# Kernel tuning notes

Measured on AMD Instinct MI355X. Metric: run time of the kernel, lower is better.

## Reference

```python
import jax, jax.numpy as jnp
import numpy as np

N, B, S = 2048, 8, 256          # nodes, graphs, nodes-per-graph (sorted equal segments)
D_IN, HID, HEADS, HC = 4096, 512, 8, 64
E, K, L, A = 32768, 8, 2, 5      # edges, rwse steps, gps layers, actions
EPS = 1e-5


def layernorm(x, g, b):
    mu = x.mean(-1, keepdims=True)
    var = ((x - mu) ** 2).mean(-1, keepdims=True)
    return (x - mu) * jax.lax.rsqrt(var + EPS) * g + b


def gelu(x):
    return jax.nn.gelu(x, approximate=False)  # torch nn.GELU default (erf)


def segment_softmax(logits, seg, num_segments):
    mx = jax.ops.segment_max(logits, seg, num_segments=num_segments)
    ex = jnp.exp(logits - mx[seg])
    den = jax.ops.segment_sum(ex, seg, num_segments=num_segments)
    return ex / (den[seg] + 1e-16)


def gatv2(h, src, dst, ea, Wl, bl, Wr, br, We, att, bias):
    # PyG GATv2Conv: x_j from lin_l(src), x_i from lin_r(dst), + lin_edge(edge_attr)
    xl = (h @ Wl + bl).reshape(N, HEADS, HC)
    xr = (h @ Wr + br).reshape(N, HEADS, HC)
    em = (ea @ We).reshape(-1, HEADS, HC)
    m = xl[src] + xr[dst] + em                     # [E+N, HEADS, HC]
    m = jnp.where(m > 0, m, 0.2 * m)               # leaky_relu(0.2)
    logit = (m * att).sum(-1)                      # [E+N, HEADS]
    alpha = segment_softmax(logit, dst, N)
    out = jax.ops.segment_sum(alpha[:, :, None] * xl[src], dst, num_segments=N)
    return out.reshape(N, HEADS * HC) + bias


def mha(xg, inW, inb, outW, outb):
    # xg: [B, S, HID]; block-diagonal per-graph attention (torch loop over batch ids)
    qkv = xg @ inW + inb
    q, k, v = jnp.split(qkv, 3, axis=-1)
    hsplit = lambda t: t.reshape(B, S, HEADS, HC).transpose(0, 2, 1, 3)
    q, k, v = hsplit(q), hsplit(k), hsplit(v)
    att = jax.nn.softmax(jnp.einsum('bhqd,bhkd->bhqk', q, k) / np.sqrt(HC), axis=-1)
    o = jnp.einsum('bhqk,bhkd->bhqd', att, v).transpose(0, 2, 1, 3).reshape(B, S, HID)
    return o @ outW + outb


def forward(x, edge_attr, rwse_W, rwse_b, rwse_g, rwse_bt, np_W, np_b, np_g, np_bt,
            gat_Wl, gat_bl, gat_Wr, gat_br, gat_We, gat_att, gat_bias,
            n1_g, n1_b, mha_inW, mha_inb, mha_outW, mha_outb, alpha_p,
            n2_g, n2_b, ffn_W1, ffn_b1, ffn_W2, ffn_b2, n3_g, n3_b,
            ah_W1, ah_b1, ah_g, ah_bt, ah_W2, ah_b2,
            edge_index, current_node_idx):
    src0, dst0 = edge_index[0], edge_index[1]
    # --- RWSE: diag of k-step random-walk transition powers ---
    adj = jnp.zeros((N, N), x.dtype).at[src0, dst0].set(1.0)
    deg = adj.sum(1, keepdims=True)
    T = adj / jnp.where(deg > 0, deg, 1.0)
    def step(cur, _):
        cur = cur @ T
        return cur, jnp.diagonal(cur)
    _, diags = jax.lax.scan(step, jnp.eye(N, dtype=x.dtype), None, length=K)
    rwse = diags.T                                  # [N, K]
    r = gelu(layernorm(rwse @ rwse_W + rwse_b, rwse_g, rwse_bt))
    h = gelu(layernorm(jnp.concatenate([x, r], -1) @ np_W + np_b, np_g, np_bt))
    # --- self loops for GATv2 (add_self_loops=True, edge_attr fill='mean') ---
    ar = jnp.arange(N)
    src = jnp.concatenate([src0, ar])
    dst = jnp.concatenate([dst0, ar])
    ea = jnp.concatenate([edge_attr, jnp.broadcast_to(edge_attr.mean(0), (N, 2))], 0)
    for i in range(L):
        local = gatv2(h, src, dst, ea, gat_Wl[i], gat_bl[i], gat_Wr[i], gat_br[i],
                      gat_We[i], gat_att[i], gat_bias[i])
        local = layernorm(local, n1_g[i], n1_b[i])
        g = mha(h.reshape(B, S, HID), mha_inW[i], mha_inb[i],
                mha_outW[i], mha_outb[i]).reshape(N, HID)
        g = layernorm(g, n2_g[i], n2_b[i])
        a = jax.nn.sigmoid(alpha_p[i])
        comb = a * local + (1.0 - a) * g
        ff = gelu(comb @ ffn_W1[i] + ffn_b1[i]) @ ffn_W2[i] + ffn_b2[i]
        h = layernorm(comb + ff, n3_g[i], n3_b[i])
    emb = h[current_node_idx]
    z = gelu(layernorm(emb @ ah_W1 + ah_b1, ah_g, ah_bt))
    logits = z @ ah_W2 + ah_b2
    return logits, jax.nn.softmax(logits, axis=-1)


def setup_inputs() -> dict:
    key = jax.random.key(0)
    ks = iter(jax.random.split(key, 64))
    def w(shape, fan_in):
        return jax.random.normal(next(ks), shape, jnp.float32) / np.sqrt(fan_in)
    H4 = HID // 4
    inp = {
        'x': jax.random.normal(next(ks), (N, D_IN), jnp.float32),
        'edge_attr': jax.random.normal(next(ks), (E, 2), jnp.float32),
        'rwse_W': w((K, H4), K), 'rwse_b': jnp.zeros(H4),
        'rwse_g': jnp.ones(H4), 'rwse_bt': jnp.zeros(H4),
        'np_W': w((D_IN + H4, HID), D_IN + H4), 'np_b': jnp.zeros(HID),
        'np_g': jnp.ones(HID), 'np_bt': jnp.zeros(HID),
        'gat_Wl': w((L, HID, HID), HID), 'gat_bl': jnp.zeros((L, HID)),
        'gat_Wr': w((L, HID, HID), HID), 'gat_br': jnp.zeros((L, HID)),
        'gat_We': w((L, 2, HID), 2), 'gat_att': w((L, HEADS, HC), HC),
        'gat_bias': jnp.zeros((L, HID)),
        'n1_g': jnp.ones((L, HID)), 'n1_b': jnp.zeros((L, HID)),
        'mha_inW': w((L, HID, 3 * HID), HID), 'mha_inb': jnp.zeros((L, 3 * HID)),
        'mha_outW': w((L, HID, HID), HID), 'mha_outb': jnp.zeros((L, HID)),
        'alpha_p': jnp.full((L,), 0.5, jnp.float32),
        'n2_g': jnp.ones((L, HID)), 'n2_b': jnp.zeros((L, HID)),
        'ffn_W1': w((L, HID, 4 * HID), HID), 'ffn_b1': jnp.zeros((L, 4 * HID)),
        'ffn_W2': w((L, 4 * HID, HID), 4 * HID), 'ffn_b2': jnp.zeros((L, HID)),
        'n3_g': jnp.ones((L, HID)), 'n3_b': jnp.zeros((L, HID)),
        'ah_W1': w((HID, HID), HID), 'ah_b1': jnp.zeros(HID),
        'ah_g': jnp.ones(HID), 'ah_bt': jnp.zeros(HID),
        'ah_W2': w((HID, A), HID), 'ah_b2': jnp.zeros(A),
        'edge_index': jax.random.randint(next(ks), (2, E), 0, N),
        'current_node_idx': 100,
    }
    return inp


def reference(x, edge_attr, rwse_W, rwse_b, rwse_g, rwse_bt, np_W, np_b, np_g, np_bt,
              gat_Wl, gat_bl, gat_Wr, gat_br, gat_We, gat_att, gat_bias,
              n1_g, n1_b, mha_inW, mha_inb, mha_outW, mha_outb, alpha_p,
              n2_g, n2_b, ffn_W1, ffn_b1, ffn_W2, ffn_b2, n3_g, n3_b,
              ah_W1, ah_b1, ah_g, ah_bt, ah_W2, ah_b2,
              edge_index, current_node_idx):
    return forward(x, edge_attr, rwse_W, rwse_b, rwse_g, rwse_bt, np_W, np_b, np_g, np_bt,
                   gat_Wl, gat_bl, gat_Wr, gat_br, gat_We, gat_att, gat_bias,
                   n1_g, n1_b, mha_inW, mha_inb, mha_outW, mha_outb, alpha_p,
                   n2_g, n2_b, ffn_W1, ffn_b1, ffn_W2, ffn_b2, n3_g, n3_b,
                   ah_W1, ah_b1, ah_g, ah_bt, ah_W2, ah_b2,
                   edge_index, current_node_idx)
```

## Files before the change

kernel.cpp:

```cpp
#include <hip/hip_runtime.h>
#include <math.h>

constexpr int NODES = 2048;
constexpr int BG = 8;
constexpr int SG = 256;
constexpr int DIN = 4096;
constexpr int NHEAD = 8;
constexpr int EDGES = 32768;
constexpr int ACT_N = 5;
constexpr int H4C = 128;
constexpr int ECAP = 192;
constexpr int SCAP = 96;
constexpr int QS = 2560;
constexpr int NC = 512;

typedef unsigned short u16;
typedef unsigned int u32;
typedef unsigned long long u64;
typedef short short8 __attribute__((ext_vector_type(8)));
typedef float f32x4 __attribute__((ext_vector_type(4)));

__device__ __forceinline__ float wave_sum(float v) {
#pragma unroll
  for (int o = 32; o; o >>= 1) v += __shfl_xor(v, o);
  return v;
}
__device__ __forceinline__ float wave_max(float v) {
#pragma unroll
  for (int o = 32; o; o >>= 1) v = fmaxf(v, __shfl_xor(v, o));
  return v;
}
__device__ __forceinline__ float blk_sum(float v, float* sh) {
  v = wave_sum(v);
  int nw = blockDim.x >> 6;
  __syncthreads();
  if ((threadIdx.x & 63) == 0) sh[threadIdx.x >> 6] = v;
  __syncthreads();
// ... 5 lines not shown
  v = wave_max(v);
  int nw = blockDim.x >> 6;
  __syncthreads();
  if ((threadIdx.x & 63) == 0) sh[threadIdx.x >> 6] = v;
  __syncthreads();
  float m = sh[0];
  for (int k = 1; k < nw; k++) m = fmaxf(m, sh[k]);
  return m;
}
__device__ __forceinline__ float gelu_f(float x) {
  return 0.5f * x * (1.f + erff(x * 0.70710678118654752f));
}
__device__ __forceinline__ u16 f2bf(float x) {
  u32 u = __float_as_uint(x);
  return (u16)((u + 0x7FFFu + ((u >> 16) & 1u)) >> 16);
}
__device__ __forceinline__ float bf2f(u16 h) { return __uint_as_float(((u32)h) << 16); }
__device__ __forceinline__ void split2(float v, u16* ph, u16* pl) {
  u16 h = f2bf(v);
  *ph = h;
  *pl = f2bf(v - bf2f(h));
}

__global__ void build_graph(const int* __restrict__ ei, u32* __restrict__ bits,
                            int* __restrict__ scnt, int* __restrict__ slist,
                            int* __restrict__ cnt, int* __restrict__ elist) {
  int e = blockIdx.x * 256 + threadIdx.x;
  if (e < EDGES) {
    int s = ei[e], d = ei[EDGES + e];
    u32 m = 1u << (d & 31);
    u32 old = atomicOr(&bits[s * 64 + (d >> 5)], m);
    if (!(old & m)) {
      int p = atomicAdd(&scnt[s], 1);
      if (p < SCAP) slist[s * SCAP + p] = d;
    }
    int p2 = atomicAdd(&cnt[d], 1);
    if (p2 < ECAP) elist[(size_t)d * ECAP + p2] = e;
  } else if (e < EDGES + NODES) {
    int d = e - EDGES;
    int p = atomicAdd(&cnt[d], 1);
    if (p < ECAP) elist[(size_t)d * ECAP + p] = e;
  }
}

__global__ __launch_bounds__(256) void spmm_sq(const int* __restrict__ scnt,
                                               const int* __restrict__ slist,
                                               float* __restrict__ P2,
                                               float* __restrict__ rwse) {
  int i = blockIdx.x, t = threadIdx.x;
  __shared__ float row[NODES];
  for (int c = t; c < NODES; c += 256) row[c] = 0.f;
  __syncthreads();
  int di = min(scnt[i], SCAP);
  float wi = di > 0 ? 1.f / (float)di : 0.f;
  for (int jj = 0; jj < di; jj++) {
    int j = slist[i * SCAP + jj];
    int dj = min(scnt[j], SCAP);
    if (dj == 0) continue;
    float w = wi / (float)dj;
    for (int kk = t; kk < dj; kk += 256) atomicAdd(&row[slist[j * SCAP + kk]], w);
  }
  __syncthreads();
  for (int c = t; c < NODES; c += 256) {
    float v = row[c];
// ... 78 lines not shown
  int self = (bits[i * 64 + (i >> 5)] >> (i & 31)) & 1;
  rwse[(size_t)i * 8 + 0] = (self && deg > 0) ? 1.f / (float)deg : 0.f;
#pragma unroll
  for (int v = 0; v < 4; v++) {
    float s = 0.f;
    for (int js = 0; js < 8; js++) s += pbuf[((size_t)js * NODES + i) * 4 + v];
    rwse[(size_t)i * 8 + 4 + v] = s;
  }
}

__device__ __forceinline__ void splitA8(const float* __restrict__ p, short8& h8,
                                        short8& l8) {
  float4 v0 = *(const float4*)p;
  float4 v1 = *(const float4*)(p + 4);
  float v[8] = {v0.x, v0.y, v0.z, v0.w, v1.x, v1.y, v1.z, v1.w};
#pragma unroll
  for (int i = 0; i < 8; i++) {
    u16 h = f2bf(v[i]);
    h8[i] = (short)h;
    l8[i] = (short)f2bf(v[i] - bf2f(h));
  }
}

__global__ void conv_split(const float* __restrict__ src, u16* __restrict__ Ah,
                           u16* __restrict__ Al, int total8, int Ksrc,
                           int dstStride, int colOff) {
  int u = blockIdx.x * 256 + threadIdx.x;
  if (u >= total8) return;
  int idx = u * 8;
  int m = idx / Ksrc, k = idx - m * Ksrc;
  short8 h8, l8;
  splitA8(src + idx, h8, l8);
  size_t o = (size_t)m * dstStride + colOff + k;
  *(short8*)(Ah + o) = h8;
  *(short8*)(Al + o) = l8;
}

struct PackArgs {
  const float* src[13];
  u64 offU[13];
  u64 cumU[14];
  int N[13];
  int srcStride[13];
  int gnTot[13];
  int ntOff[13];
};

__global__ __launch_bounds__(256) void pack_all(PackArgs pa, u16* __restrict__ Bh,
                                                u16* __restrict__ Bl) {
  u64 total = pa.cumU[13];
  for (u64 u = (u64)blockIdx.x * 256 + threadIdx.x; u < total;
       u += (u64)gridDim.x * 256) {
    int s = 0;
    while (u >= pa.cumU[s + 1]) s++;
    u64 ur = u - pa.cumU[s];
    int lr = (int)(ur & 15);
    int g = (int)((ur >> 4) & 3);
    int ks = (int)((ur >> 6) & 1);
    int j = (int)((ur >> 7) & 3);
    u64 rest = ur >> 9;
    int Nseg = pa.N[s] >> 6;
    int nt = (int)(rest % (u32)Nseg);
    int ktile = (int)(rest / (u32)Nseg);
    int k0 = (ktile << 6) | (ks << 5) | (g << 3);
    int n = (nt << 6) | (j << 4) | lr;
    const float* src = pa.src[s];
    int stride = pa.srcStride[s];
    u64 fiU = pa.offU[s] +
              ((((u64)ktile * pa.gnTot[s] + pa.ntOff[s] + nt) * 8 + j * 2 + ks) * 64 +
               g * 16 + lr);
    short8 h8, l8;
#pragma unroll
    for (int e = 0; e < 8; e++) {
      float v = src[(size_t)(k0 + e) * stride + n];
      u16 h = f2bf(v);
      h8[e] = (short)h;
      l8[e] = (short)f2bf(v - bf2f(h));
    }
// ... 177 lines not shown
    v1 += x[(size_t)s * MN + base + 256 + t];
  }
  if (gbias) { v0 += gbias[t]; v1 += gbias[t + 256]; }
  if (res) { v0 += res[base + t]; v1 += res[base + 256 + t]; }
  __shared__ float sh[8];
  float s = blk_sum(v0 + v1, sh);
  float mu = s * (1.f / 512.f);
  float d0 = v0 - mu, d1 = v1 - mu;
  float var = blk_sum(d0 * d0 + d1 * d1, sh) * (1.f / 512.f);
  float rstd = rsqrtf(var + 1e-5f);
  float o0 = d0 * rstd * g[t] + b[t];
  float o1 = d1 * rstd * g[t + 256] + b[t + 256];
  if (do_gelu) { o0 = gelu_f(o0); o1 = gelu_f(o1); }
  if (mix) {
    float a = 1.f / (1.f + expf(-ap[l]));
    o0 = a * mix[base + t] + (1.f - a) * o0;
    o1 = a * mix[base + 256 + t] + (1.f - a) * o1;
  }
  if (y) { y[base + t] = o0; y[base + 256 + t] = o1; }
  if (yh) {
    split2(o0, yh + base + t, yl + base + t);
    split2(o1, yh + base + 256 + t, yl + base + 256 + t);
  }
}

__global__ void build_cbias(const float* __restrict__ bl, const float* __restrict__ br,
                            const float* __restrict__ inb, float* __restrict__ cb) {
  int i = blockIdx.x * 256 + threadIdx.x;
  if (i >= QS) return;
  cb[i] = i < 512 ? bl[i] : (i < 1024 ? br[i - 512] : inb[i - 1024]);
}

__global__ void build_rowmap(const int* __restrict__ cni, const int* __restrict__ cnt,
                             const int* __restrict__ elist, const int* __restrict__ ei,
                             int* __restrict__ rowmap) {
  int t = blockIdx.x * 256 + threadIdx.x;
  if (t >= NC) return;
  int i = cni[0];
  if (t < 256) {
    rowmap[t] = ((i >> 8) << 8) + t;
  } else {
    int p = t - 256;
    int m = min(cnt[i], ECAP);
    int v = 0;
    if (p < m) {
      int eid = elist[(size_t)i * ECAP + p];
      v = eid < EDGES ? ei[eid] : i;
    }
    rowmap[t] = v;
  }
}

__global__ void ea_reduce(const float* __restrict__ ea, float* __restrict__ sums) {
  int tid = blockIdx.x * blockDim.x + threadIdx.x;
  int stride = gridDim.x * blockDim.x;
  float s0 = 0.f, s1 = 0.f;
  for (int e = tid; e < EDGES; e += stride) { s0 += ea[2 * e]; s1 += ea[2 * e + 1]; }
  s0 = wave_sum(s0);
  s1 = wave_sum(s1);
  if ((threadIdx.x & 63) == 0) { atomicAdd(&sums[0], s0); atomicAdd(&sums[1], s1); }
}

__global__ __launch_bounds__(512) void gat_kernel(
    const float* __restrict__ hb, const int* __restrict__ rowmap,
    const float* __restrict__ eattr, const float* __restrict__ easum,
    const float* __restrict__ We, const float* __restrict__ att,
    const float* __restrict__ bias, const int* __restrict__ cnt,
    const int* __restrict__ elist, const int* __restrict__ ei,
    const float* __restrict__ n1g, const float* __restrict__ n1b,
    float* __restrict__ out) {
  int i = rowmap[blockIdx.x];
  int tid = threadIdx.x;
  int h = tid >> 6, c = tid & 63;
  int m_cnt = cnt[i];
  if (m_cnt > ECAP) m_cnt = ECAP;
  const float inv_e = 1.f / (float)EDGES;
  float we0 = We[tid], we1 = We[512 + tid];
  float attv = att[tid];
  float xrv = hb[(size_t)i * QS + 512 + tid];
  float ea_m0 = easum[0] * inv_e, ea_m1 = easum[1] * inv_e;
  __shared__ float logits[NHEAD][ECAP];
  __shared__ float sh[8];
  const int* el = elist + (size_t)i * ECAP;
// ... 174 lines not shown
  int kb = blockIdx.y;
  const float* xr = h1c + (size_t)(cni[0] & 255) * 512 + kb * 64;
  if (t < 64) xv[t] = xr[t];
  __syncthreads();
  int b = blockIdx.x;
  int isq = b < 8;
  int nl = t & 63;
  int n = (b & 7) * 64 + nl;
  int seg = t >> 6;
  const float* W = isq ? inW : Wr;
  int ldW = isq ? 1536 : 512;
  float acc = 0.f;
  const float* Wp = W + (size_t)(kb * 64 + seg * 16) * ldW + n;
#pragma unroll
  for (int k = 0; k < 16; k++) acc += xv[seg * 16 + k] * Wp[(size_t)k * ldW];
  red[seg][nl] = acc;
  __syncthreads();
  if (t < 64) {
    part[(size_t)kb * 1024 + (isq ? 0 : 512) + (b & 7) * 64 + t] =
        red[0][t] + red[1][t] + red[2][t] + red[3][t];
  }
}

__global__ void reduce_qxr(const float* __restrict__ part,
                           const float* __restrict__ inb,
                           const float* __restrict__ br,
                           float* __restrict__ qrow, float* __restrict__ xrrow) {
  int n = blockIdx.x * 256 + threadIdx.x;
  float s = n < 512 ? inb[n] : br[n - 512];
  for (int k = 0; k < 8; k++) s += part[(size_t)k * 1024 + n];
  if (n < 512) qrow[n] = s;
  else xrrow[n - 512] = s;
}

__global__ void row_reduce(const float* __restrict__ part, int KB, int N,
                           const float* __restrict__ bias,
                           float* __restrict__ out, int act) {
  int n = blockIdx.x * 256 + threadIdx.x;
  if (n >= N) return;
  float s = bias[n];
  for (int k = 0; k < KB; k++) s += part[(size_t)k * N + n];
  if (act) s = gelu_f(s);
  out[n] = s;
}

__global__ __launch_bounds__(512) void gat_l2(
    const float* __restrict__ xlc, const float* __restrict__ xrrow,
    const int* __restrict__ cni,
    const float* __restrict__ eattr, const float* __restrict__ easum,
    const float* __restrict__ We, const float* __restrict__ att,
    const float* __restrict__ bias, const int* __restrict__ cnt,
    const int* __restrict__ elist,
    const float* __restrict__ n1g, const float* __restrict__ n1b,
    float* __restrict__ local_row) {
  int i = cni[0];
  int tid = threadIdx.x;
  int h = tid >> 6, c = tid & 63;
  int m_cnt = cnt[i];
  if (m_cnt > ECAP) m_cnt = ECAP;
  const float inv_e = 1.f / (float)EDGES;
  float we0 = We[tid], we1 = We[512 + tid];
  float attv = att[tid];
  float xrv = xrrow[tid];
  float ea_m0 = easum[0] * inv_e, ea_m1 = easum[1] * inv_e;
  __shared__ float logits[NHEAD][ECAP];
  __shared__ float sh[8];
  const int* el = elist + (size_t)i * ECAP;
  for (int e = 0; e < m_cnt; e++) {
    int eid = el[e];
    float a0, a1;
    if (eid < EDGES) { a0 = eattr[2 * eid]; a1 = eattr[2 * eid + 1]; }
    else { a0 = ea_m0; a1 = ea_m1; }
    float mval = xlc[(size_t)(256 + e) * 512 + tid] + xrv + a0 * we0 + a1 * we1;
    mval = mval > 0.f ? mval : 0.2f * mval;
    float lg = wave_sum(mval * attv);
    if (c == 0) logits[h][e] = lg;
  }
  float mx = -1e30f;
  for (int e = c; e < m_cnt; e += 64) mx = fmaxf(mx, logits[h][e]);
  mx = wave_max(mx);
  float den = 0.f;
  for (int e = c; e < m_cnt; e += 64) den += expf(logits[h][e] - mx);
  den = wave_sum(den) + 1e-16f;
  float acc = 0.f;
  for (int e = 0; e < m_cnt; e++) {
    float alpha = expf(logits[h][e] - mx) / den;
    acc += alpha * xlc[(size_t)(256 + e) * 512 + tid];
  }
  float v = acc + bias[tid];
  float mu = blk_sum(v, sh) * (1.f / 512.f);
  float d = v - mu;
  float var = blk_sum(d * d, sh) * (1.f / 512.f);
  local_row[tid] = d * rsqrtf(var + 1e-5f) * n1g[tid] + n1b[tid];
}

__global__ __launch_bounds__(256) void mha_row(const float* __restrict__ qrow,
                                               const float* __restrict__ kv,
                                               float* __restrict__ attO_row) {
  __shared__ float q[64];
  __shared__ float p[SG];
  __shared__ float sh[8];
  __shared__ float red[4][64];
  int h = blockIdx.x, t = threadIdx.x;
  if (t < 64) q[t] = qrow[h * 64 + t];
  __syncthreads();
  const float* kr = kv + (size_t)t * 1024 + h * 64;
  float s = 0.f;
#pragma unroll 8
  for (int c2 = 0; c2 < 64; c2++) s += q[c2] * kr[c2];
  s *= 0.125f;
  float m = blk_max(s, sh);
  float e = __expf(s - m);
  p[t] = e;
  float den = blk_sum(e, sh);
  int c = t & 63, seg = t >> 6;
  float o = 0.f;
  for (int j = seg * 64; j < seg * 64 + 64; j++)
    o += p[j] * kv[(size_t)j * 1024 + 512 + h * 64 + c];
  red[seg][c] = o;
  __syncthreads();
  if (t < 64)
    attO_row[h * 64 + t] = (red[0][t] + red[1][t] + red[2][t] + red[3][t]) / den;
}

__global__ __launch_bounds__(512) void comb_l2(const float* __restrict__ part, int KB,
                                               const float* __restrict__ bias,
                                               const float* __restrict__ local_row,
                                               const float* __restrict__ ap, int l,
                                               const float* __restrict__ g,
                                               const float* __restrict__ b,
                                               float* __restrict__ comb_row) {
  __shared__ float sh[8];
  int t = threadIdx.x;
  float v = bias[t];
  for (int k = 0; k < KB; k++) v += part[(size_t)k * 512 + t];
  float mu = blk_sum(v, sh) * (1.f / 512.f);
  float d = v - mu;
  float var = blk_sum(d * d, sh) * (1.f / 512.f);
  float o = d * rsqrtf(var + 1e-5f) * g[t] + b[t];
  float a = 1.f / (1.f + expf(-ap[l]));
  comb_row[t] = a * local_row[t] + (1.f - a) * o;
}

__global__ __launch_bounds__(512) void final_l2(const float* __restrict__ part, int KB,
                                                const float* __restrict__ bias,
                                                const float* __restrict__ comb_row,
                                                const float* __restrict__ g,
                                                const float* __restrict__ b,
                                                float* __restrict__ hrow) {
  __shared__ float sh[8];
  int t = threadIdx.x;
  float v = bias[t] + comb_row[t];
  for (int k = 0; k < KB; k++) v += part[(size_t)k * 512 + t];
  float mu = blk_sum(v, sh) * (1.f / 512.f);
  float d = v - mu;
  float var = blk_sum(d * d, sh) * (1.f / 512.f);
  hrow[t] = d * rsqrtf(var + 1e-5f) * g[t] + b[t];
}

__global__ __launch_bounds__(512) void head_finish(
    const float* __restrict__ part, int KB,
    const float* __restrict__ b1,
    const float* __restrict__ g, const float* __restrict__ bt,
    const float* __restrict__ W2, const float* __restrict__ b2,
    float* __restrict__ out) {
  __shared__ float sh[8];
  __shared__ float lg[ACT_N];
  int t = threadIdx.x;
  float v = b1[t];
  for (int k = 0; k < KB; k++) v += part[(size_t)k * 512 + t];
  float mu = blk_sum(v, sh) * (1.f / 512.f);
  float d = v - mu;
  float var = blk_sum(d * d, sh) * (1.f / 512.f);
  float z = gelu_f(d * rsqrtf(var + 1e-5f) * g[t] + bt[t]);
  for (int a = 0; a < ACT_N; a++) {
    float s = blk_sum(z * W2[t * ACT_N + a], sh);
    if (t == 0) lg[a] = s + b2[a];
  }
  __syncthreads();
  if (t == 0) {
// ... 53 lines not shown
  const int* edge_index = (const int*)d_in[38];
  const int* cni        = (const int*)d_in[39];
  (void)in_sizes; (void)n_in; (void)out_size; (void)ws_size;

  char* wsp = (char*)d_ws;
  size_t off = 0;
  auto alloc = [&](size_t bytes) -> char* {
    char* p = wsp + off;
    off += (bytes + 255) & ~(size_t)255;
    return p;
  };
  const size_t NNb = (size_t)NODES * NODES * 4;
  char* arena = alloc(3 * NNb);
  float* P2 = (float*)arena;
  float* P3 = (float*)(arena + NNb);
  float* P4 = (float*)(arena + 2 * NNb);
  u16* Axh = (u16*)arena;
  u16* Axl = (u16*)(arena + 17301504);
  float* hbig = (float*)arena;
  float* partC = (float*)(arena + 22020096);
  const u64 SEG_NP = 2162688ull;
  const u64 SEG_L0 = 3670016ull;
  const u64 L1_OFF = SEG_NP + SEG_L0;
  const u64 KV1_OFF = L1_OFF + 262144ull;
  const u64 PTOT = KV1_OFF + 524288ull;
  u16* Bh = (u16*)alloc(PTOT * 2);
  u16* Bl = (u16*)alloc(PTOT * 2);
  float* partNP = (float*)alloc((size_t)6 * NODES * 512 * 4);
  float* rwse = (float*)alloc((size_t)NODES * 8 * 4);
  u16* h1h = (u16*)alloc((size_t)NODES * 512 * 2);
  u16* h1l = (u16*)alloc((size_t)NODES * 512 * 2);
  u16* attOh = (u16*)alloc((size_t)NODES * 512 * 2);
  u16* attOl = (u16*)alloc((size_t)NODES * 512 * 2);
  u16* combh = (u16*)alloc((size_t)NC * 512 * 2);
  u16* combl = (u16*)alloc((size_t)NC * 512 * 2);
  u16* ffmh = (u16*)alloc((size_t)NC * 2048 * 2);
  u16* ffml = (u16*)alloc((size_t)NC * 2048 * 2);
  u16* h1ch = (u16*)alloc((size_t)NC * 512 * 2);
  u16* h1cl = (u16*)alloc((size_t)NC * 512 * 2);
  float* h1c  = (float*)alloc((size_t)NC * 512 * 4);
  float* gout = (float*)alloc((size_t)NC * 512 * 4);
  float* comb = (float*)alloc((size_t)NC * 512 * 4);
  float* kvbuf = (float*)alloc((size_t)256 * 1024 * 4);
  float* cb   = (float*)alloc((size_t)QS * 4);
  float* rows = (float*)alloc(4096 * 4);
  float* pv1 = (float*)alloc((size_t)32 * 2048 * 4);
  char* zbase = alloc((size_t)NODES * 64 * 4 + NODES * 4 + NODES * 4 + 256);
  u32* bits  = (u32*)zbase;
  int* scnt  = (int*)(zbase + (size_t)NODES * 64 * 4);
  int* cnt   = (int*)(zbase + (size_t)NODES * 64 * 4 + NODES * 4);
  float* easum = (float*)(zbase + (size_t)NODES * 64 * 4 + NODES * 8);
  size_t zbytes = (size_t)NODES * 64 * 4 + NODES * 8 + 256;
  int* slist = (int*)alloc((size_t)NODES * SCAP * 4);
  int* elist = (int*)alloc((size_t)NODES * ECAP * 4);
  int* rmap  = (int*)alloc((size_t)NC * 4);
  float* pbuf  = (float*)alloc((size_t)8 * NODES * 4 * 4);
  float* qrow = rows, *xrrow = rows + 512, *local_row = rows + 1024;
  float* attO_row = rows + 1536, *comb_row = rows + 2560;
  float* midrow = rows + 3072 - 1024;
  float* midrow2 = (float*)alloc(2048 * 4);
  float* hrow = rows + 3584;

  hipMemsetAsync(zbase, 0, zbytes, stream);
  build_graph<<<(EDGES + NODES + 255) / 256, 256, 0, stream>>>(edge_index, bits,
                                                               scnt, slist, cnt,
                                                               elist);
  ea_reduce<<<64, 256, 0, stream>>>(eattr, easum);
  build_rowmap<<<2, 256, 0, stream>>>(cni, cnt, elist, edge_index, rmap);

  spmm_sq<<<NODES, 256, 0, stream>>>(scnt, slist, P2, rwse);
  spmm_gather<<<NODES, 256, 0, stream>>>(scnt, slist, P2, P3, rwse, 2);
  spmm_gather<<<NODES, 256, 0, stream>>>(scnt, slist, P3, P4, rwse, 3);
  diag_tiled<<<dim3(NODES / 64, 8), 256, 0, stream>>>(P2, P3, P4, pbuf);
  diag_reduce<<<NODES / 256, 256, 0, stream>>>(pbuf, bits, scnt, rwse);
  conv_split<<<NODES * DIN / 8 / 256, 256, 0, stream>>>(x, Axh, Axl,
                                                        NODES * DIN / 8, DIN, 4224, 0);
  rwse_proj<<<NODES, 128, 0, stream>>>(rwse, rwse_W, rwse_b, rwse_g, rwse_bt,
                                       Axh, Axl);

  PackArgs pa;
  u64 uc = 0;
  int si = 0;
  auto seg = [&](const float* src, int K, int N, int stride, u64 offElems,
                 int gnTot, int ntOff) {
    pa.src[si] = src; pa.offU[si] = offElems / 8; pa.cumU[si] = uc;
    pa.N[si] = N; pa.srcStride[si] = stride; pa.gnTot[si] = gnTot;
    pa.ntOff[si] = ntOff;
    uc += (u64)K * N / 8; si++;
  };
  seg(np_W, 4224, 512, 512, 0, 8, 0);
  seg(gat_Wl, 512, 512, 512, SEG_NP, 40, 0);
  seg(gat_Wr, 512, 512, 512, SEG_NP, 40, 8);
  seg(mha_inW, 512, 1536, 1536, SEG_NP, 40, 16);
  seg(mha_outW, 512, 512, 512, SEG_NP + 1310720, 8, 0);
  seg(ffn_W1, 512, 2048, 2048, SEG_NP + 1572864, 32, 0);
  seg(ffn_W2, 2048, 512, 512, SEG_NP + 2621440, 8, 0);
  seg(gat_Wl + 512 * 512, 512, 512, 512, L1_OFF, 8, 0);
  seg(mha_inW + 512 * 1536 + 512, 512, 1024, 1536, KV1_OFF, 16, 0);
  for (int s2 = si; s2 <= 13; s2++) pa.cumU[s2] = uc;
  pack_all<<<2048, 256, 0, stream>>>(pa, Bh, Bl);
  build_cbias<<<(QS + 255) / 256, 256, 0, stream>>>(gat_bl, gat_br, mha_inb, cb);

  gemm_s<<<dim3(256, 6), 256, 0, stream>>>(Axh, Axl, 4224, Bh, Bl,
                                           nullptr, nullptr, nullptr, nullptr,
                                           NODES, 4224, 512, 0, 704, partNP,
                                           nullptr);
  ln512<<<NODES, 256, 0, stream>>>(partNP, 6, NODES, np_b, nullptr, nullptr,
                                   nullptr, 0, np_g, np_bt, nullptr, h1h, h1l, 1);

  {
    const u64 lb = SEG_NP;
    gemm_s<<<dim3(1280), 256, 0, stream>>>(h1h, h1l, 512, Bh + lb, Bl + lb,
                                           hbig, nullptr, nullptr, cb,
                                           NODES, 512, QS, 0, 512, nullptr,
                                           nullptr);
    gat_kernel<<<NC, 512, 0, stream>>>(hbig, rmap, eattr, easum, gat_We, gat_att,
                                       gat_bias, cnt, elist, edge_index,
                                       n1_g, n1_b, gout);
    mha_mfma<<<BG * NHEAD * 4, 256, 0, stream>>>(hbig + 1024, attOh, attOl);
    gemm_s<<<dim3(64, 2), 256, 0, stream>>>(attOh, attOl, 512, Bh + lb + 1310720,
                                            Bl + lb + 1310720, nullptr, nullptr,
                                            nullptr, nullptr, NC, 512, 512, 0, 256,
                                            partC, rmap);
    ln512<<<NC, 256, 0, stream>>>(partC, 2, NC, mha_outb, nullptr, gout, alpha_p,
                                  0, n2_g, n2_b, comb, combh, combl, 0);
    gemm_s<<<dim3(256), 256, 0, stream>>>(combh, combl, 512, Bh + lb + 1572864,
                                          Bl + lb + 1572864, nullptr, ffmh, ffml,
                                          ffn_b1, NC, 512, 2048, 1, 512, nullptr,
                                          nullptr);
    gemm_s<<<dim3(64, 4), 256, 0, stream>>>(ffmh, ffml, 2048, Bh + lb + 2621440,
                                            Bl + lb + 2621440, nullptr, nullptr,
                                            nullptr, nullptr, NC, 2048, 512, 0,
                                            512, partC, nullptr);
    ln512<<<NC, 256, 0, stream>>>(partC, 4, NC, ffn_b2, comb, nullptr, nullptr, 0,
                                  n3_g, n3_b, h1c, h1ch, h1cl, 0);
  }

  {
    float* xlc = gout;
    gemm_s<<<dim3(64), 256, 0, stream>>>(h1ch, h1cl, 512, Bh + L1_OFF, Bl + L1_OFF,
                                         xlc, nullptr, nullptr, gat_bl + 512,
                                         NC, 512, 512, 0, 512, nullptr, nullptr);
    gemm_s<<<dim3(64), 256, 0, stream>>>(h1ch, h1cl, 512, Bh + KV1_OFF, Bl + KV1_OFF,
                                         kvbuf, nullptr, nullptr,
                                         mha_inb + 1536 + 512, 256, 512, 1024, 0,
                                         512, nullptr, nullptr);
    gemv_qxr<<<dim3(16, 8), 256, 0, stream>>>(h1c, cni, mha_inW + 512 * 1536,
                                              gat_Wr + 512 * 512, pv1);
    reduce_qxr<<<4, 256, 0, stream>>>(pv1, mha_inb + 1536, gat_br + 512, qrow,
                                      xrrow);
    gat_l2<<<1, 512, 0, stream>>>(xlc, xrrow, cni, eattr, easum, gat_We + 1024,
                                  gat_att + 512, gat_bias + 512, cnt, elist,
                                  n1_g + 512, n1_b + 512, local_row);
    mha_row<<<8, 256, 0, stream>>>(qrow, kvbuf, attO_row);
    gemv_part<<<dim3(8, 8), 256, 0, stream>>>(attO_row, nullptr, 0, 0,
                                              mha_outW + 512 * 512, 512, 512, pv1);
    comb_l2<<<1, 512, 0, stream>>>(pv1, 8, mha_outb + 512, local_row, alpha_p, 1,
                                   n2_g + 512, n2_b + 512, comb_row);
    gemv_part<<<dim3(32, 8), 256, 0, stream>>>(comb_row, nullptr, 0, 0,
                                               ffn_W1 + (size_t)512 * 2048, 2048,
                                               2048, pv1);
    row_reduce<<<8, 256, 0, stream>>>(pv1, 8, 2048, ffn_b1 + 2048, midrow2, 1);
    gemv_part<<<dim3(8, 32), 256, 0, stream>>>(midrow2, nullptr, 0, 0,
                                               ffn_W2 + (size_t)2048 * 512, 512,
                                               512, pv1);
    final_l2<<<1, 512, 0, stream>>>(pv1, 32, ffn_b2 + 512, comb_row, n3_g + 512,
                                    n3_b + 512, hrow);
  }

  gemv_part<<<dim3(8, 8), 256, 0, stream>>>(hrow, nullptr, 0, 0, ah_W1, 512, 512,
                                            pv1);
  head_finish<<<1, 512, 0, stream>>>(pv1, 8, ah_b1, ah_g, ah_bt, ah_W2, ah_b2,
                                     (float*)d_out);
  (void)midrow;
}
```

Measured before the change: 400.8 us.

## Fuse small setup, layer-2 attention and GEMV reduce kernels to cut launch count

Folds the edge-attribute sum into build_graph, merges rowmap and bias setup into one kernel, and moves the x bf16 split into pack_all. In layer 2 it merges the xl and KV GEMMs into one wider GEMM, fuses GAT and MHA row attention into a single launch, and folds each partial-sum reduction and layernorm into the following GEMV. The aim is to remove many tiny serial launches and intermediate round trips; in exchange, each fused GEMV block redundantly recomputes the layernorm and reduction.

```diff
diff --git a/kernel.cpp b/kernel.cpp
--- a/kernel.cpp
+++ b/kernel.cpp
@@ -13,6 +13,7 @@
 constexpr int SCAP = 96;
 constexpr int QS = 2560;
 constexpr int NC = 512;
+constexpr int XK = 1536;
 
 typedef unsigned short u16;
 typedef unsigned int u32;
@@ -64,10 +65,13 @@
   *pl = f2bf(v - bf2f(h));
 }
 
-__global__ void build_graph(const int* __restrict__ ei, u32* __restrict__ bits,
+__global__ void build_graph(const int* __restrict__ ei, const float* __restrict__ ea,
+                            u32* __restrict__ bits,
                             int* __restrict__ scnt, int* __restrict__ slist,
-                            int* __restrict__ cnt, int* __restrict__ elist) {
+                            int* __restrict__ cnt, int* __restrict__ elist,
+                            float* __restrict__ sums) {
   int e = blockIdx.x * 256 + threadIdx.x;
+  float s0 = 0.f, s1 = 0.f;
   if (e < EDGES) {
     int s = ei[e], d = ei[EDGES + e];
     u32 m = 1u << (d & 31);
@@ -78,10 +82,49 @@
     }
     int p2 = atomicAdd(&cnt[d], 1);
     if (p2 < ECAP) elist[(size_t)d * ECAP + p2] = e;
+    s0 = ea[2 * e];
+    s1 = ea[2 * e + 1];
   } else if (e < EDGES + NODES) {
     int d = e - EDGES;
     int p = atomicAdd(&cnt[d], 1);
     if (p < ECAP) elist[(size_t)d * ECAP + p] = e;
+  }
+  s0 = wave_sum(s0);
+  s1 = wave_sum(s1);
+  if ((threadIdx.x & 63) == 0 && (s0 != 0.f || s1 != 0.f)) {
+    atomicAdd(&sums[0], s0);
+    atomicAdd(&sums[1], s1);
+  }
+}
+
+__global__ void small_setup(const int* __restrict__ cni, const int* __restrict__ cnt,
+                            const int* __restrict__ elist, const int* __restrict__ ei,
+                            int* __restrict__ rowmap,
+                            const float* __restrict__ bl0, const float* __restrict__ br0,
+                            const float* __restrict__ inb0, float* __restrict__ cb,
+                            const float* __restrict__ bl1, const float* __restrict__ inb1,
+                            float* __restrict__ cbX) {
+  int t = blockIdx.x * 256 + threadIdx.x;
+  if (t < NC) {
+    int i = cni[0];
+    if (t < 256) {
+      rowmap[t] = ((i >> 8) << 8) + t;
+    } else {
+      int p = t - 256;
+      int m = min(cnt[i], ECAP);
+      int v = 0;
+      if (p < m) {
+        int eid = elist[(size_t)i * ECAP + p];
+        v = eid < EDGES ? ei[eid] : i;
+      }
+      rowmap[t] = v;
+    }
+  } else if (t < NC + QS) {
+    int i = t - NC;
+    cb[i] = i < 512 ? bl0[i] : (i < 1024 ? br0[i - 512] : inb0[i - 1024]);
+  } else if (t < NC + QS + XK) {
+    int i = t - NC - QS;
+    cbX[i] = i < 512 ? bl1[i] : inb1[i];
   }
 }
 
@@ -206,20 +249,6 @@
   }
 }
 
-__global__ void conv_split(const float* __restrict__ src, u16* __restrict__ Ah,
-                           u16* __restrict__ Al, int total8, int Ksrc,
-                           int dstStride, int colOff) {
-  int u = blockIdx.x * 256 + threadIdx.x;
-  if (u >= total8) return;
-  int idx = u * 8;
-  int m = idx / Ksrc, k = idx - m * Ksrc;
-  short8 h8, l8;
-  splitA8(src + idx, h8, l8);
-  size_t o = (size_t)m * dstStride + colOff + k;
-  *(short8*)(Ah + o) = h8;
-  *(short8*)(Al + o) = l8;
-}
-
 struct PackArgs {
   const float* src[13];
   u64 offU[13];
@@ -231,13 +260,25 @@
 };
 
 __global__ __launch_bounds__(256) void pack_all(PackArgs pa, u16* __restrict__ Bh,
-                                                u16* __restrict__ Bl) {
+                                                u16* __restrict__ Bl,
+                                                u16* __restrict__ Axh,
+                                                u16* __restrict__ Axl) {
   u64 total = pa.cumU[13];
   for (u64 u = (u64)blockIdx.x * 256 + threadIdx.x; u < total;
        u += (u64)gridDim.x * 256) {
     int s = 0;
     while (u >= pa.cumU[s + 1]) s++;
     u64 ur = u - pa.cumU[s];
+    if (pa.gnTot[s] < 0) {
+      int m = (int)(ur >> 9);
+      int k = (int)((ur & 511) << 3);
+      short8 h8, l8;
+      splitA8(pa.src[s] + (size_t)m * 4096 + k, h8, l8);
+      size_t o = (size_t)m * 4224 + k;
+      *(short8*)(Axh + o) = h8;
+      *(short8*)(Axl + o) = l8;
+      continue;
+    }
     int lr = (int)(ur & 15);
     int g = (int)((ur >> 4) & 3);
     int ks = (int)((ur >> 6) & 1);
@@ -461,43 +502,6 @@
     split2(o0, yh + base + t, yl + base + t);
     split2(o1, yh + base + 256 + t, yl + base + 256 + t);
   }
-}
-
-__global__ void build_cbias(const float* __restrict__ bl, const float* __restrict__ br,
-                            const float* __restrict__ inb, float* __restrict__ cb) {
-  int i = blockIdx.x * 256 + threadIdx.x;
-  if (i >= QS) return;
-  cb[i] = i < 512 ? bl[i] : (i < 1024 ? br[i - 512] : inb[i - 1024]);
-}
-
-__global__ void build_rowmap(const int* __restrict__ cni, const int* __restrict__ cnt,
-                             const int* __restrict__ elist, const int* __restrict__ ei,
-                             int* __restrict__ rowmap) {
-  int t = blockIdx.x * 256 + threadIdx.x;
-  if (t >= NC) return;
-  int i = cni[0];
-  if (t < 256) {
-    rowmap[t] = ((i >> 8) << 8) + t;
-  } else {
-    int p = t - 256;
-    int m = min(cnt[i], ECAP);
-    int v = 0;
-    if (p < m) {
-      int eid = elist[(size_t)i * ECAP + p];
-      v = eid < EDGES ? ei[eid] : i;
-    }
-    rowmap[t] = v;
-  }
-}
-
-__global__ void ea_reduce(const float* __restrict__ ea, float* __restrict__ sums) {
-  int tid = blockIdx.x * blockDim.x + threadIdx.x;
-  int stride = gridDim.x * blockDim.x;
-  float s0 = 0.f, s1 = 0.f;
-  for (int e = tid; e < EDGES; e += stride) { s0 += ea[2 * e]; s1 += ea[2 * e + 1]; }
-  s0 = wave_sum(s0);
-  s1 = wave_sum(s1);
-  if ((threadIdx.x & 63) == 0) { atomicAdd(&sums[0], s0); atomicAdd(&sums[1], s1); }
 }
 
 __global__ __launch_bounds__(512) void gat_kernel(
@@ -718,140 +722,199 @@
   }
 }
 
-__global__ void reduce_qxr(const float* __restrict__ part,
-                           const float* __restrict__ inb,
-                           const float* __restrict__ br,
-                           float* __restrict__ qrow, float* __restrict__ xrrow) {
-  int n = blockIdx.x * 256 + threadIdx.x;
-  float s = n < 512 ? inb[n] : br[n - 512];
-  for (int k = 0; k < 8; k++) s += part[(size_t)k * 1024 + n];
-  if (n < 512) qrow[n] = s;
-  else xrrow[n - 512] = s;
-}
-
-__global__ void row_reduce(const float* __restrict__ part, int KB, int N,
-                           const float* __restrict__ bias,
-                           float* __restrict__ out, int act) {
-  int n = blockIdx.x * 256 + threadIdx.x;
-  if (n >= N) return;
-  float s = bias[n];
-  for (int k = 0; k < KB; k++) s += part[(size_t)k * N + n];
-  if (act) s = gelu_f(s);
-  out[n] = s;
-}
-
-__global__ __launch_bounds__(512) void gat_l2(
-    const float* __restrict__ xlc, const float* __restrict__ xrrow,
+__global__ __launch_bounds__(512) void l2_attn(
+    const float* __restrict__ xkc, const float* __restrict__ pvqxr,
     const int* __restrict__ cni,
     const float* __restrict__ eattr, const float* __restrict__ easum,
     const float* __restrict__ We, const float* __restrict__ att,
     const float* __restrict__ bias, const int* __restrict__ cnt,
     const int* __restrict__ elist,
     const float* __restrict__ n1g, const float* __restrict__ n1b,
-    float* __restrict__ local_row) {
-  int i = cni[0];
-  int tid = threadIdx.x;
-  int h = tid >> 6, c = tid & 63;
-  int m_cnt = cnt[i];
-  if (m_cnt > ECAP) m_cnt = ECAP;
-  const float inv_e = 1.f / (float)EDGES;
-  float we0 = We[tid], we1 = We[512 + tid];
-  float attv = att[tid];
-  float xrv = xrrow[tid];
-  float ea_m0 = easum[0] * inv_e, ea_m1 = easum[1] * inv_e;
+    const float* __restrict__ inbq, const float* __restrict__ br,
+    float* __restrict__ local_row, float* __restrict__ attO_row) {
   __shared__ float logits[NHEAD][ECAP];
   __shared__ float sh[8];
-  const int* el = elist + (size_t)i * ECAP;
-  for (int e = 0; e < m_cnt; e++) {
-    int eid = el[e];
-    float a0, a1;
-    if (eid < EDGES) { a0 = eattr[2 * eid]; a1 = eattr[2 * eid + 1]; }
-    else { a0 = ea_m0; a1 = ea_m1; }
-    float mval = xlc[(size_t)(256 + e) * 512 + tid] + xrv + a0 * we0 + a1 * we1;
-    mval = mval > 0.f ? mval : 0.2f * mval;
-    float lg = wave_sum(mval * attv);
-    if (c == 0) logits[h][e] = lg;
-  }
-  float mx = -1e30f;
-  for (int e = c; e < m_cnt; e += 64) mx = fmaxf(mx, logits[h][e]);
-  mx = wave_max(mx);
-  float den = 0.f;
-  for (int e = c; e < m_cnt; e += 64) den += expf(logits[h][e] - mx);
-  den = wave_sum(den) + 1e-16f;
-  float acc = 0.f;
-  for (int e = 0; e < m_cnt; e++) {
-    float alpha = expf(logits[h][e] - mx) / den;
-    acc += alpha * xlc[(size_t)(256 + e) * 512 + tid];
-  }
-  float v = acc + bias[tid];
-  float mu = blk_sum(v, sh) * (1.f / 512.f);
-  float d = v - mu;
-  float var = blk_sum(d * d, sh) * (1.f / 512.f);
-  local_row[tid] = d * rsqrtf(var + 1e-5f) * n1g[tid] + n1b[tid];
-}
-
-__global__ __launch_bounds__(256) void mha_row(const float* __restrict__ qrow,
-                                               const float* __restrict__ kv,
-                                               float* __restrict__ attO_row) {
   __shared__ float q[64];
   __shared__ float p[SG];
+  __shared__ float red[8][64];
+  if (blockIdx.x == 0) {
+    int i = cni[0];
+    int tid = threadIdx.x;
+    int h = tid >> 6, c = tid & 63;
+    int m_cnt = min(cnt[i], ECAP);
+    const float inv_e = 1.f / (float)EDGES;
+    float we0 = We[tid], we1 = We[512 + tid];
+    float attv = att[tid];
+    float xrv = br[tid];
+    for (int k = 0; k < 8; k++) xrv += pvqxr[(size_t)k * 1024 + 512 + tid];
+    float ea_m0 = easum[0] * inv_e, ea_m1 = easum[1] * inv_e;
+    const int* el = elist + (size_t)i * ECAP;
+    for (int e = 0; e < m_cnt; e++) {
+      int eid = el[e];
+      float a0, a1;
+      if (eid < EDGES) { a0 = eattr[2 * eid]; a1 = eattr[2 * eid + 1]; }
+      else { a0 = ea_m0; a1 = ea_m1; }
+      float mval = xkc[(size_t)(256 + e) * XK + tid] + xrv + a0 * we0 + a1 * we1;
+      mval = mval > 0.f ? mval : 0.2f * mval;
+      float lg = wave_sum(mval * attv);
+      if (c == 0) logits[h][e] = lg;
+    }
+    float mx = -1e30f;
+    for (int e = c; e < m_cnt; e += 64) mx = fmaxf(mx, logits[h][e]);
+    mx = wave_max(mx);
+    float den = 0.f;
+    for (int e = c; e < m_cnt; e += 64) den += expf(logits[h][e] - mx);
+    den = wave_sum(den) + 1e-16f;
+    float acc = 0.f;
+    for (int e = 0; e < m_cnt; e++) {
+      float alpha = expf(logits[h][e] - mx) / den;
+      acc += alpha * xkc[(size_t)(256 + e) * XK + tid];
+    }
+    float v = acc + bias[tid];
+    float mu = blk_sum(v, sh) * (1.f / 512.f);
+    float d = v - mu;
+    float var = blk_sum(d * d, sh) * (1.f / 512.f);
+    local_row[tid] = d * rsqrtf(var + 1e-5f) * n1g[tid] + n1b[tid];
+  } else {
+    int h = blockIdx.x - 1;
+    int t = threadIdx.x;
+    if (t < 64) {
+      float qq = inbq[h * 64 + t];
+      for (int k = 0; k < 8; k++) qq += pvqxr[(size_t)k * 1024 + h * 64 + t];
+      q[t] = qq;
+    }
+    __syncthreads();
+    float s = -1e30f;
+    if (t < SG) {
+      const float* kr = xkc + (size_t)t * XK + 512 + h * 64;
+      float acc = 0.f;
+#pragma unroll 8
+      for (int c2 = 0; c2 < 64; c2++) acc += q[c2] * kr[c2];
+      s = acc * 0.125f;
+    }
+    float m = blk_max(s, sh);
+    float e2 = (t < SG) ? __expf(s - m) : 0.f;
+    if (t < SG) p[t] = e2;
+    float den = blk_sum(e2, sh);
+    __syncthreads();
+    int c = t & 63, seg = t >> 6;
+    float o = 0.f;
+    for (int j = seg * 32; j < seg * 32 + 32; j++)
+      o += p[j] * xkc[(size_t)j * XK + 1024 + h * 64 + c];
+    red[seg][c] = o;
+    __syncthreads();
+    if (t < 64) {
+      float tot = 0.f;
+      for (int k = 0; k < 8; k++) tot += red[k][t];
+      attO_row[h * 64 + t] = tot / den;
+    }
+  }
+}
+
+__global__ __launch_bounds__(256) void gemv_comb(
+    const float* __restrict__ pvout, const float* __restrict__ outb,
+    const float* __restrict__ local_row, const float* __restrict__ ap,
+    const float* __restrict__ n2g, const float* __restrict__ n2b,
+    const float* __restrict__ W, float* __restrict__ comb_out,
+    float* __restrict__ part) {
+  __shared__ float combs[512];
   __shared__ float sh[8];
   __shared__ float red[4][64];
-  int h = blockIdx.x, t = threadIdx.x;
-  if (t < 64) q[t] = qrow[h * 64 + t];
-  __syncthreads();
-  const float* kr = kv + (size_t)t * 1024 + h * 64;
-  float s = 0.f;
-#pragma unroll 8
-  for (int c2 = 0; c2 < 64; c2++) s += q[c2] * kr[c2];
-  s *= 0.125f;
-  float m = blk_max(s, sh);
-  float e = __expf(s - m);
-  p[t] = e;
-  float den = blk_sum(e, sh);
-  int c = t & 63, seg = t >> 6;
-  float o = 0.f;
-  for (int j = seg * 64; j < seg * 64 + 64; j++)
-    o += p[j] * kv[(size_t)j * 1024 + 512 + h * 64 + c];
-  red[seg][c] = o;
+  int t = threadIdx.x;
+  float v0 = outb[t], v1 = outb[t + 256];
+  for (int k = 0; k < 8; k++) {
+    v0 += pvout[(size_t)k * 512 + t];
+    v1 += pvout[(size_t)k * 512 + 256 + t];
+  }
+  float ssum = blk_sum(v0 + v1, sh);
+  float mu = ssum * (1.f / 512.f);
+  float d0 = v0 - mu, d1 = v1 - mu;
+  float var = blk_sum(d0 * d0 + d1 * d1, sh) * (1.f / 512.f);
+  float rstd = rsqrtf(var + 1e-5f);
+  float o0 = d0 * rstd * n2g[t] + n2b[t];
+  float o1 = d1 * rstd * n2g[t + 256] + n2b[t + 256];
+  float a = 1.f / (1.f + expf(-ap[1]));
+  combs[t] = a * local_row[t] + (1.f - a) * o0;
+  combs[t + 256] = a * local_row[t + 256] + (1.f - a) * o1;
+  __syncthreads();
+  if (blockIdx.x == 0 && blockIdx.y == 0) {
+    comb_out[t] = combs[t];
+    comb_out[t + 256] = combs[t + 256];
+  }
+  int kb = blockIdx.y;
+  int nl = t & 63, seg = t >> 6;
+  int n = blockIdx.x * 64 + nl;
+  float acc = 0.f;
+  const float* Wp = W + (size_t)(kb * 64 + seg * 16) * 2048 + n;
+#pragma unroll
+  for (int k = 0; k < 16; k++) acc += combs[kb * 64 + seg * 16 + k] * Wp[(size_t)k * 2048];
+  red[seg][nl] = acc;
   __syncthreads();
   if (t < 64)
-    attO_row[h * 64 + t] = (red[0][t] + red[1][t] + red[2][t] + red[3][t]) / den;
-}
-
-__global__ __launch_bounds__(512) void comb_l2(const float* __restrict__ part, int KB,
-                                               const float* __restrict__ bias,
-                                               const float* __restrict__ local_row,
-                                               const float* __restrict__ ap, int l,
-                                               const float* __restrict__ g,
-                                               const float* __restrict__ b,
-                                               float* __restrict__ comb_row) {
+    part[(size_t)kb * 2048 + blockIdx.x * 64 + t] =
+        red[0][t] + red[1][t] + red[2][t] + red[3][t];
+}
+
+__global__ __launch_bounds__(256) void gemv_mid(
+    const float* __restrict__ pvW1, const float* __restrict__ b1,
+    const float* __restrict__ W, float* __restrict__ part) {
+  __shared__ float xv[64];
+  __shared__ float red[4][64];
+  int t = threadIdx.x;
+  int kb = blockIdx.y;
+  if (t < 64) {
+    float s = b1[kb * 64 + t];
+    for (int k = 0; k < 8; k++) s += pvW1[(size_t)k * 2048 + kb * 64 + t];
+    xv[t] = gelu_f(s);
+  }
+  __syncthreads();
+  int nl = t & 63, seg = t >> 6;
+  int n = blockIdx.x * 64 + nl;
+  float acc = 0.f;
+  const float* Wp = W + (size_t)(kb * 64 + seg * 16) * 512 + n;
+#pragma unroll
+  for (int k = 0; k < 16; k++) acc += xv[seg * 16 + k] * Wp[(size_t)k * 512];
+  red[seg][nl] = acc;
+  __syncthreads();
+  if (t < 64)
+    part[(size_t)kb * 512 + blockIdx.x * 64 + t] =
+        red[0][t] + red[1][t] + red[2][t] + red[3][t];
+}
+
+__global__ __launch_bounds__(256) void gemv_head(
+    const float* __restrict__ pvW2, const float* __restrict__ b2,
+    const float* __restrict__ comb_row,
+    const float* __restrict__ n3g, const float* __restrict__ n3b,
+    const float* __restrict__ W, float* __restrict__ part) {
+  __shared__ float hr[512];
   __shared__ float sh[8];
+  __shared__ float red[4][64];
   int t = threadIdx.x;
-  float v = bias[t];
-  for (int k = 0; k < KB; k++) v += part[(size_t)k * 512 + t];
-  float mu = blk_sum(v, sh) * (1.f / 512.f);
-  float d = v - mu;
-  float var = blk_sum(d * d, sh) * (1.f / 512.f);
-  float o = d * rsqrtf(var + 1e-5f) * g[t] + b[t];
-  float a = 1.f / (1.f + expf(-ap[l]));
-  comb_row[t] = a * local_row[t] + (1.f - a) * o;
-}
-
-__global__ __launch_bounds__(512) void final_l2(const float* __restrict__ part, int KB,
-                                                const float* __restrict__ bias,
-                                                const float* __restrict__ comb_row,
-                                                const float* __restrict__ g,
-                                                const float* __restrict__ b,
-                                                float* __restrict__ hrow) {
-  __shared__ float sh[8];
-  int t = threadIdx.x;
-  float v = bias[t] + comb_row[t];
-  for (int k = 0; k < KB; k++) v += part[(size_t)k * 512 + t];
-  float mu = blk_sum(v, sh) * (1.f / 512.f);
-  float d = v - mu;
-  float var = blk_sum(d * d, sh) * (1.f / 512.f);
-  hrow[t] = d * rsqrtf(var + 1e-5f) * g[t] + b[t];
+  float v0 = b2[t] + comb_row[t], v1 = b2[t + 256] + comb_row[t + 256];
+  for (int k = 0; k < 32; k++) {
+    v0 += pvW2[(size_t)k * 512 + t];
+    v1 += pvW2[(size_t)k * 512 + 256 + t];
+  }
+  float ssum = blk_sum(v0 + v1, sh);
+  float mu = ssum * (1.f / 512.f);
+  float d0 = v0 - mu, d1 = v1 - mu;
+  float var = blk_sum(d0 * d0 + d1 * d1, sh) * (1.f / 512.f);
+  float rstd = rsqrtf(var + 1e-5f);
+  hr[t] = d0 * rstd * n3g[t] + n3b[t];
+  hr[t + 256] = d1 * rstd * n3g[t + 256] + n3b[t + 256];
+  __syncthreads();
+  int kb = blockIdx.y;
+  int nl = t & 63, seg = t >> 6;
+  int n = blockIdx.x * 64 + nl;
+  float acc = 0.f;
+  const float* Wp = W + (size_t)(kb * 64 + seg * 16) * 512 + n;
+#pragma unroll
+  for (int k = 0; k < 16; k++) acc += hr[kb * 64 + seg * 16 + k] * Wp[(size_t)k * 512];
+  red[seg][nl] = acc;
+  __syncthreads();
+  if (t < 64)
+    part[(size_t)kb * 512 + blockIdx.x * 64 + t] =
+        red[0][t] + red[1][t] + red[2][t] + red[3][t];
 }
 
 __global__ __launch_bounds__(512) void head_finish(
@@ -951,8 +1014,7 @@
   const u64 SEG_NP = 2162688ull;
   const u64 SEG_L0 = 3670016ull;
   const u64 L1_OFF = SEG_NP + SEG_L0;
-  const u64 KV1_OFF = L1_OFF + 262144ull;
-  const u64 PTOT = KV1_OFF + 524288ull;
+  const u64 PTOT = L1_OFF + 786432ull;
   u16* Bh = (u16*)alloc(PTOT * 2);
   u16* Bl = (u16*)alloc(PTOT * 2);
   float* partNP = (float*)alloc((size_t)6 * NODES * 512 * 4);
@@ -970,10 +1032,15 @@
   float* h1c  = (float*)alloc((size_t)NC * 512 * 4);
   float* gout = (float*)alloc((size_t)NC * 512 * 4);
   float* comb = (float*)alloc((size_t)NC * 512 * 4);
-  float* kvbuf = (float*)alloc((size_t)256 * 1024 * 4);
+  float* xkc  = (float*)alloc((size_t)NC * XK * 4);
   float* cb   = (float*)alloc((size_t)QS * 4);
+  float* cbX  = (float*)alloc((size_t)XK * 4);
   float* rows = (float*)alloc(4096 * 4);
-  float* pv1 = (float*)alloc((size_t)32 * 2048 * 4);
+  float* pvqxr = (float*)alloc((size_t)8 * 1024 * 4);
+  float* pvout = (float*)alloc((size_t)8 * 512 * 4);
+  float* pvW1  = (float*)alloc((size_t)8 * 2048 * 4);
+  float* pvW2  = (float*)alloc((size_t)32 * 512 * 4);
+  float* pvhd  = (float*)alloc((size_t)8 * 512 * 4);
   char* zbase = alloc((size_t)NODES * 64 * 4 + NODES * 4 + NODES * 4 + 256);
   u32* bits  = (u32*)zbase;
   int* scnt  = (int*)(zbase + (size_t)NODES * 64 * 4);
@@ -984,28 +1051,22 @@
   int* elist = (int*)alloc((size_t)NODES * ECAP * 4);
   int* rmap  = (int*)alloc((size_t)NC * 4);
   float* pbuf  = (float*)alloc((size_t)8 * NODES * 4 * 4);
-  float* qrow = rows, *xrrow = rows + 512, *local_row = rows + 1024;
-  float* attO_row = rows + 1536, *comb_row = rows + 2560;
-  float* midrow = rows + 3072 - 1024;
-  float* midrow2 = (float*)alloc(2048 * 4);
-  float* hrow = rows + 3584;
+  float* local_row = rows + 1024;
+  float* attO_row = rows + 1536;
+  float* comb_row = rows + 2560;
 
   hipMemsetAsync(zbase, 0, zbytes, stream);
-  build_graph<<<(EDGES + NODES + 255) / 256, 256, 0, stream>>>(edge_index, bits,
-                                                               scnt, slist, cnt,
-                                                               elist);
-  ea_reduce<<<64, 256, 0, stream>>>(eattr, easum);
-  build_rowmap<<<2, 256, 0, stream>>>(cni, cnt, elist, edge_index, rmap);
+  build_graph<<<(EDGES + NODES + 255) / 256, 256, 0, stream>>>(
+      edge_index, eattr, bits, scnt, slist, cnt, elist, easum);
+  small_setup<<<(NC + QS + XK + 255) / 256, 256, 0, stream>>>(
+      cni, cnt, elist, edge_index, rmap, gat_bl, gat_br, mha_inb, cb,
+      gat_bl + 512, mha_inb + 1536, cbX);
 
   spmm_sq<<<NODES, 256, 0, stream>>>(scnt, slist, P2, rwse);
   spmm_gather<<<NODES, 256, 0, stream>>>(scnt, slist, P2, P3, rwse, 2);
   spmm_gather<<<NODES, 256, 0, stream>>>(scnt, slist, P3, P4, rwse, 3);
   diag_tiled<<<dim3(NODES / 64, 8), 256, 0, stream>>>(P2, P3, P4, pbuf);
   diag_reduce<<<NODES / 256, 256, 0, stream>>>(pbuf, bits, scnt, rwse);
-  conv_split<<<NODES * DIN / 8 / 256, 256, 0, stream>>>(x, Axh, Axl,
-                                                        NODES * DIN / 8, DIN, 4224, 0);
-  rwse_proj<<<NODES, 128, 0, stream>>>(rwse, rwse_W, rwse_b, rwse_g, rwse_bt,
-                                       Axh, Axl);
 
   PackArgs pa;
   u64 uc = 0;
@@ -1024,11 +1085,13 @@
   seg(mha_outW, 512, 512, 512, SEG_NP + 1310720, 8, 0);
   seg(ffn_W1, 512, 2048, 2048, SEG_NP + 1572864, 32, 0);
   seg(ffn_W2, 2048, 512, 512, SEG_NP + 2621440, 8, 0);
-  seg(gat_Wl + 512 * 512, 512, 512, 512, L1_OFF, 8, 0);
-  seg(mha_inW + 512 * 1536 + 512, 512, 1024, 1536, KV1_OFF, 16, 0);
+  seg(gat_Wl + 512 * 512, 512, 512, 512, L1_OFF, 24, 0);
+  seg(mha_inW + 512 * 1536 + 512, 512, 1024, 1536, L1_OFF, 24, 8);
+  seg(x, NODES, 4096, 4096, 0, -1, 0);
   for (int s2 = si; s2 <= 13; s2++) pa.cumU[s2] = uc;
-  pack_all<<<2048, 256, 0, stream>>>(pa, Bh, Bl);
-  build_cbias<<<(QS + 255) / 256, 256, 0, stream>>>(gat_bl, gat_br, mha_inb, cb);
+  pack_all<<<4096, 256, 0, stream>>>(pa, Bh, Bl, Axh, Axl);
+  rwse_proj<<<NODES, 128, 0, stream>>>(rwse, rwse_W, rwse_b, rwse_g, rwse_bt,
+                                       Axh, Axl);
 
   gemm_s<<<dim3(256, 6), 256, 0, stream>>>(Axh, Axl, 4224, Bh, Bl,
                                            nullptr, nullptr, nullptr, nullptr,
@@ -1066,40 +1129,29 @@
   }
 
   {
-    float* xlc = gout;
-    gemm_s<<<dim3(64), 256, 0, stream>>>(h1ch, h1cl, 512, Bh + L1_OFF, Bl + L1_OFF,
-                                         xlc, nullptr, nullptr, gat_bl + 512,
-                                         NC, 512, 512, 0, 512, nullptr, nullptr);
-    gemm_s<<<dim3(64), 256, 0, stream>>>(h1ch, h1cl, 512, Bh + KV1_OFF, Bl + KV1_OFF,
-                                         kvbuf, nullptr, nullptr,
-                                         mha_inb + 1536 + 512, 256, 512, 1024, 0,
-                                         512, nullptr, nullptr);
+    gemm_s<<<dim3(192), 256, 0, stream>>>(h1ch, h1cl, 512, Bh + L1_OFF,
+                                          Bl + L1_OFF, xkc, nullptr, nullptr,
+                                          cbX, NC, 512, XK, 0, 512, nullptr,
+                                          nullptr);
     gemv_qxr<<<dim3(16, 8), 256, 0, stream>>>(h1c, cni, mha_inW + 512 * 1536,
-                                              gat_Wr + 512 * 512, pv1);
-    reduce_qxr<<<4, 256, 0, stream>>>(pv1, mha_inb + 1536, gat_br + 512, qrow,
-                                      xrrow);
-    gat_l2<<<1, 512, 0, stream>>>(xlc, xrrow, cni, eattr, easum, gat_We + 1024,
-                                  gat_att + 512, gat_bias + 512, cnt, elist,
-                                  n1_g + 512, n1_b + 512, local_row);
-    mha_row<<<8, 256, 0, stream>>>(qrow, kvbuf, attO_row);
+                                              gat_Wr + 512 * 512, pvqxr);
+    l2_attn<<<9, 512, 0, stream>>>(xkc, pvqxr, cni, eattr, easum, gat_We + 1024,
+                                   gat_att + 512, gat_bias + 512, cnt, elist,
+                                   n1_g + 512, n1_b + 512, mha_inb + 1536,
+                                   gat_br + 512, local_row, attO_row);
     gemv_part<<<dim3(8, 8), 256, 0, stream>>>(attO_row, nullptr, 0, 0,
-                                              mha_outW + 512 * 512, 512, 512, pv1);
-    comb_l2<<<1, 512, 0, stream>>>(pv1, 8, mha_outb + 512, local_row, alpha_p, 1,
-                                   n2_g + 512, n2_b + 512, comb_row);
-    gemv_part<<<dim3(32, 8), 256, 0, stream>>>(comb_row, nullptr, 0, 0,
-                                               ffn_W1 + (size_t)512 * 2048, 2048,
-                                               2048, pv1);
-    row_reduce<<<8, 256, 0, stream>>>(pv1, 8, 2048, ffn_b1 + 2048, midrow2, 1);
-    gemv_part<<<dim3(8, 32), 256, 0, stream>>>(midrow2, nullptr, 0, 0,
-                                               ffn_W2 + (size_t)2048 * 512, 512,
-                                               512, pv1);
-    final_l2<<<1, 512, 0, stream>>>(pv1, 32, ffn_b2 + 512, comb_row, n3_g + 512,
-                                    n3_b + 512, hrow);
-  }
-
-  gemv_part<<<dim3(8, 8), 256, 0, stream>>>(hrow, nullptr, 0, 0, ah_W1, 512, 512,
-                                            pv1);
-  head_finish<<<1, 512, 0, stream>>>(pv1, 8, ah_b1, ah_g, ah_bt, ah_W2, ah_b2,
-                                     (float*)d_out);
-  (void)midrow;
-}
+                                              mha_outW + 512 * 512, 512, 512,
+                                              pvout);
+    gemv_comb<<<dim3(32, 8), 256, 0, stream>>>(pvout, mha_outb + 512, local_row,
+                                               alpha_p, n2_g + 512, n2_b + 512,
+                                               ffn_W1 + (size_t)512 * 2048,
+                                               comb_row, pvW1);
+    gemv_mid<<<dim3(8, 32), 256, 0, stream>>>(pvW1, ffn_b1 + 2048,
+                                              ffn_W2 + (size_t)2048 * 512, pvW2);
+    gemv_head<<<dim3(8, 8), 256, 0, stream>>>(pvW2, ffn_b2 + 512, comb_row,
+                                              n3_g + 512, n3_b + 512, ah_W1,
+                                              pvhd);
+    head_finish<<<1, 512, 0, stream>>>(pvhd, 8, ah_b1, ah_g, ah_bt, ah_W2, ah_b2,
+                                       (float*)d_out);
+  }
+}
```

Result: faster. 357.8 us (-10.7%).
